# Kernel optimization log

Measured on AMD Instinct MI355X. Metric: run time of the kernel, lower is better.

Reference implementation:

```python
import jax, jax.numpy as jnp
import numpy as np

# ---- config (mirrors argparse-config of dnc_model) ----
T, B, IN = 64, 32, 64          # time-major input [T,B,IN]
N, Wd, R, NW = 512, 64, 4, 1   # memory_size, word_size, num_reads, num_writes
H, OUT = 256, 64               # controller hidden, output_size
CLIP = 20.0
EPS = 1e-6
IF = R*Wd + R + NW*Wd + NW + NW*Wd + NW*Wd + R + NW + NW + R*(1+2*NW)  # interface size = 471
CTRL_IN = IN + R*Wd


def setup_inputs() -> dict:
    key = jax.random.key(0)
    ks = jax.random.split(key, 6)
    g = lambda k, shape, s: (jax.random.normal(k, shape, jnp.float32) * s)
    return {
        "inputs": g(ks[0], (T, B, IN), 1.0),
        "Wx": g(ks[1], (CTRL_IN, 4*H), 0.05),
        "Wh": g(ks[2], (H, 4*H), 0.05),
        "b_lstm": jnp.zeros((4*H,), jnp.float32),
        "W_if": g(ks[3], (H, IF), 0.05),
        "b_if": jnp.zeros((IF,), jnp.float32),
        "W_out": g(ks[4], (H + R*Wd, OUT), 0.05),
        "b_out": jnp.zeros((OUT,), jnp.float32),
    }


def _clip(x):
    return jnp.clip(x, -CLIP, CLIP)


def _oneplus(x):
    return 1.0 + jax.nn.softplus(x)


def _content_weights(memory, keys, strengths):
    # memory [B,N,Wd], keys [B,K,Wd], strengths [B,K] -> softmax cosine weights [B,K,N]
    dot = jnp.einsum('bkw,bnw->bkn', keys, memory)
    mn = jnp.sqrt(jnp.sum(memory * memory, -1))          # [B,N]
    kn = jnp.sqrt(jnp.sum(keys * keys, -1))              # [B,K]
    sim = dot / (kn[..., None] * mn[:, None, :] + EPS)
    return jax.nn.softmax(sim * strengths[..., None], axis=-1)


def _allocation(usage):
    # usage [B,N] -> allocation weights [B,N] (sorted-free-list scheme)
    u = EPS + (1.0 - EPS) * usage
    idx = jnp.argsort(u, axis=-1)                        # ascending usage
    su = jnp.take_along_axis(u, idx, -1)
    cp = jnp.cumprod(su, axis=-1)
    excl = jnp.concatenate([jnp.ones_like(cp[:, :1]), cp[:, :-1]], -1)
    a_sorted = (1.0 - su) * excl
    inv = jnp.argsort(idx, axis=-1)
    return jnp.take_along_axis(a_sorted, inv, -1)


def _dnc_forward(inputs, Wx, Wh, b_lstm, W_if, b_if, W_out, b_out):
    eye = jnp.eye(N, dtype=inputs.dtype)

    def step(carry, x_t):
        h, c, mem, rw, ww_prev, link, prec, usage, reads = carry
        # ---- controller LSTM (prev read vectors fed in) ----
        ctrl_in = jnp.concatenate([x_t, reads.reshape(B, R*Wd)], -1)
        gates = ctrl_in @ Wx + h @ Wh + b_lstm
        ig, fg, gg, og = jnp.split(gates, 4, -1)
        c = jax.nn.sigmoid(fg) * c + jax.nn.sigmoid(ig) * jnp.tanh(gg)
        h = jax.nn.sigmoid(og) * jnp.tanh(c)
        hc, cc = _clip(h), _clip(c)
        # ---- interface vector ----
        itf = hc @ W_if + b_if
        off = 0
        read_keys = itf[:, off:off+R*Wd].reshape(B, R, Wd); off += R*Wd
        read_str = _oneplus(itf[:, off:off+R]); off += R
        write_keys = itf[:, off:off+NW*Wd].reshape(B, NW, Wd); off += NW*Wd
        write_str = _oneplus(itf[:, off:off+NW]); off += NW
        erase = jax.nn.sigmoid(itf[:, off:off+NW*Wd]).reshape(B, NW, Wd); off += NW*Wd
        write_vecs = itf[:, off:off+NW*Wd].reshape(B, NW, Wd); off += NW*Wd
        free_g = jax.nn.sigmoid(itf[:, off:off+R]); off += R
        alloc_g = jax.nn.sigmoid(itf[:, off:off+NW]); off += NW
        write_g = jax.nn.sigmoid(itf[:, off:off+NW]); off += NW
        modes = jax.nn.softmax(itf[:, off:off+R*(1+2*NW)].reshape(B, R, 1+2*NW), -1)
        bwd_mode = modes[..., :NW]
        fwd_mode = modes[..., NW:2*NW]
        content_mode = modes[..., 2*NW]
        # ---- usage update (uses prev write/read weights) ----
        u = usage + (1.0 - usage) * (1.0 - jnp.prod(1.0 - ww_prev, axis=1))
        psi = jnp.prod(1.0 - free_g[..., None] * rw, axis=1)
        usage = u * psi
        # ---- write weights: allocation + content ----
        allocs = []
        u_run = usage
        for hd in range(NW):
            a = _allocation(u_run)
            allocs.append(a)
            u_run = u_run + (1.0 - u_run) * (write_g[:, hd:hd+1] * alloc_g[:, hd:hd+1]) * a
        alloc = jnp.stack(allocs, 1)                      # [B,NW,N]
        wc = _content_weights(mem, write_keys, write_str) # [B,NW,N]
        ww = write_g[..., None] * (alloc_g[..., None] * alloc + (1.0 - alloc_g[..., None]) * wc)
        # ---- erase / add write ----
        erase_w = ww[..., None] * erase[:, :, None, :]    # [B,NW,N,Wd]
        mem = mem * jnp.prod(1.0 - erase_w, axis=1) + jnp.einsum('bhn,bhw->bnw', ww, write_vecs)
        # ---- temporal link + precedence ----
        w_i = ww[..., :, None]
        w_j = ww[..., None, :]
        link = (1.0 - w_i - w_j) * link + w_i * prec[..., None, :]
        link = link * (1.0 - eye)
        prec = (1.0 - ww.sum(-1, keepdims=True)) * prec + ww
        # ---- read weights: content + forward/backward linkage ----
        rc = _content_weights(mem, read_keys, read_str)   # [B,R,N]
        fw = jnp.einsum('bhij,brj->brhi', link, rw)       # forward  [B,R,NW,N]
        bw = jnp.einsum('bhji,brj->brhi', link, rw)       # backward [B,R,NW,N]
        rw = (content_mode[..., None] * rc
              + jnp.einsum('brh,brhn->brn', fwd_mode, fw)
              + jnp.einsum('brh,brhn->brn', bwd_mode, bw))
        reads = jnp.einsum('brn,bnw->brw', rw, mem)       # [B,R,Wd]
        out = _clip(jnp.concatenate([hc, reads.reshape(B, R*Wd)], -1) @ W_out + b_out)
        return (hc, cc, mem, rw, ww, link, prec, usage, reads), out

    z = jnp.zeros
    dt = inputs.dtype
    carry0 = (z((B, H), dt), z((B, H), dt), z((B, N, Wd), dt), z((B, R, N), dt),
              z((B, NW, N), dt), z((B, NW, N, N), dt), z((B, NW, N), dt),
              z((B, N), dt), z((B, R, Wd), dt))
    _, outs = jax.lax.scan(step, carry0, inputs)
    return outs  # [T, B, OUT]


def reference(inputs, Wx, Wh, b_lstm, W_if, b_if, W_out, b_out):
    return _dnc_forward(inputs, Wx, Wh, b_lstm, W_if, b_if, W_out, b_out)
```

## Files before the change

kernel.cpp:

```cpp
#include <hip/hip_runtime.h>
#include <math.h>

#define Tn 64
#define Bn 32
#define INn 64
#define Nn 512
#define WDn 64
#define Rn 4
#define Hn 256
#define G4H 1024
#define OUTn 64
#define IFn 471
#define CLIPV 20.0f
#define EPSV 1e-6f

#define OFF_RKEY 0
#define OFF_RSTR 256
#define OFF_WKEY 260
#define OFF_WSTR 324
#define OFF_ERASE 325
#define OFF_WVEC 389
#define OFF_FREE 453
#define OFF_AG 457
#define OFF_WG 458
#define OFF_MODES 459

__device__ float S_h[2][Bn][Hn];
__device__ float S_c[2][Bn][Hn];
__device__ float S_gates[2][Bn][G4H];
__device__ float S_mem[Bn][Nn][WDn];
__device__ float S_rw[Bn][Rn][Nn];
__device__ float S_ww[2][Bn][Nn];
__device__ float S_link[Bn][Nn][Nn];
__device__ float S_prec[2][Bn][Nn];
__device__ float S_usage[2][Bn][Nn];
__device__ float S_reads[Bn][Rn][WDn];
__device__ float S_itf[Bn][IFn];
__device__ float S_wsim[Bn][Nn];
__device__ float S_fw[Bn][Rn][Nn];
__device__ float S_bwp[Bn][8][Rn*Nn];
__device__ float S_sumww[Bn];
__device__ unsigned int g_hh[16];
__device__ unsigned int g_hb[Bn][16];
__device__ unsigned int g_itf[Bn][16];
__device__ unsigned int g_sim[Bn][16];
__device__ unsigned int g_ww[Bn][16];
__device__ unsigned int g_ld[Bn][16];
__device__ unsigned int g_fin[16];

__device__ __forceinline__ float sigm(float x){ return 1.f/(1.f+expf(-x)); }
__device__ __forceinline__ float clipv(float x){ return fminf(fmaxf(x,-CLIPV),CLIPV); }
__device__ __forceinline__ float oneplusf(float x){
  float sp = (x > 0.f) ? (x + log1pf(expf(-x))) : log1pf(expf(x));
  return 1.f + sp;
}
__device__ __forceinline__ float wredsum(float v){
  #pragma unroll
  for (int o=32;o>0;o>>=1) v += __shfl_xor(v,o,64);
  return v;
}
__device__ __forceinline__ float bredsum(float v, volatile float* scr){
  v = wredsum(v);
  if ((threadIdx.x & 63) == 0) scr[threadIdx.x >> 6] = v;
  __syncthreads();
  float s = scr[0];
  #pragma unroll
  for (int i=1;i<8;i++) s += scr[i];
  __syncthreads();
  return s;
}
__device__ __forceinline__ float bredmax(float v, volatile float* scr){
  #pragma unroll
  for (int o=32;o>0;o>>=1) v = fmaxf(v,__shfl_xor(v,o,64));
  if ((threadIdx.x & 63) == 0) scr[threadIdx.x >> 6] = v;
  __syncthreads();
  float m = scr[0];
  #pragma unroll
  for (int i=1;i<8;i++) m = fmaxf(m, scr[i]);
  __syncthreads();
  return m;
}
__device__ __forceinline__ void sig_release(unsigned int* flag){
  __builtin_amdgcn_fence(__ATOMIC_RELEASE, "agent");
  __hip_atomic_fetch_add(flag, 1u, __ATOMIC_RELAXED, __HIP_MEMORY_SCOPE_AGENT);
}
__device__ __forceinline__ void spin_until(unsigned int* flag, unsigned int target){
  while (__hip_atomic_load(flag, __ATOMIC_RELAXED, __HIP_MEMORY_SCOPE_AGENT) < target)
    __builtin_amdgcn_s_sleep(1);
}
__device__ __forceinline__ void wait_acq1(unsigned int* f, unsigned int tgt){
  if (threadIdx.x==0){
    spin_until(f, tgt);
    __builtin_amdgcn_fence(__ATOMIC_ACQUIRE, "agent");
  }
  __syncthreads();
}

extern "C" __global__ void __launch_bounds__(256)
k_init(){
  size_t g = (size_t)blockIdx.x*256 + threadIdx.x;
  size_t stride = (size_t)gridDim.x*256;
  float* lk = &S_link[0][0][0];
  for (size_t i=g; i<(size_t)Bn*Nn*Nn; i+=stride) lk[i]=0.f;
  float* mm = &S_mem[0][0][0];
  for (size_t i=g; i<(size_t)Bn*Nn*WDn; i+=stride) mm[i]=0.f;
  float* rr = &S_rw[0][0][0];
  for (size_t i=g; i<(size_t)Bn*Rn*Nn; i+=stride) rr[i]=0.f;
  float* rd = &S_reads[0][0][0];
  for (size_t i=g; i<(size_t)Bn*Rn*WDn; i+=stride) rd[i]=0.f;
  for (size_t i=g; i<(size_t)2*Bn*Nn; i+=stride){
    S_ww[0][0][i]=0.f; S_prec[0][0][i]=0.f; S_usage[0][0][i]=0.f;
  }
  for (size_t i=g; i<(size_t)2*Bn*Hn; i+=stride){
    S_h[0][0][i]=0.f; S_c[0][0][i]=0.f;
  }
  if (blockIdx.x==0){
    for (int i=threadIdx.x; i<16; i+=256){ g_hh[i]=0u; g_fin[i]=0u; }
    for (int i=threadIdx.x; i<Bn*16; i+=256){
      ((unsigned int*)g_hb)[i]=0u; ((unsigned int*)g_itf)[i]=0u;
      ((unsigned int*)g_sim)[i]=0u; ((unsigned int*)g_ww)[i]=0u;
      ((unsigned int*)g_ld)[i]=0u;
    }
  }
}

struct ShG { float ctrl[Bn][65]; };
struct ShAF {
  float itf[IFn];
  float ww[Nn];
  float red[8];
  float betar[Rn], knr[Rn], modes[Rn][4];
  float er[WDn], wv[WDn], rk[Rn][WDn];
  union {
    struct { unsigned long long keys[Nn]; float alloc[Nn]; float wsim[Nn]; } pre;
    struct {
      float tile[64][65];
      float rsim[Rn][Nn];
      float fw[Rn][Nn];
      float bw[Rn][Nn];
      float part[8][Rn][WDn];
      float vin[512];
    } post;
  } u;
};
struct ShL {
  float hc[Hn];
  float ipart[8][64];
  float wkey[WDn];
  float knw, betaw;
  float ww[Nn];
  float prec[Nn];
  float rw[Rn][Nn];
  float bwp4[4][Rn][Nn];
};
union ShU { ShAF a; ShL l; ShG g; };

extern "C" __global__ void __launch_bounds__(512)
k_gates_pro(const float* __restrict__ xin, const float* __restrict__ Wx,
            const float* __restrict__ Wh, const float* __restrict__ b_lstm){
  __shared__ ShG sg;
  const int tid = threadIdx.x, lane = tid & 63, wvi = tid >> 6;
  const int j = blockIdx.x*64 + lane;
  const int b0 = wvi*4;
  float bias = b_lstm[j];
  float a0=bias, a1=bias, a2=bias, a3=bias;
  {
    #pragma unroll
    for (int u=0;u<4;u++){
      int e = u*512 + tid;
      int b2 = e >> 6, kk = e & 63;
      sg.ctrl[b2][kk] = xin[(size_t)b2*INn + kk];
    }
    __syncthreads();
    const float* wb = Wx + j;
    #pragma unroll
    for (int kk=0;kk<64;kk++){
      float wv = wb[(size_t)kk*G4H];
      a0 += sg.ctrl[b0+0][kk]*wv;
      a1 += sg.ctrl[b0+1][kk]*wv;
      a2 += sg.ctrl[b0+2][kk]*wv;
      a3 += sg.ctrl[b0+3][kk]*wv;
    }
  }
  S_gates[0][b0+0][j]=a0;
  S_gates[0][b0+1][j]=a1;
  S_gates[0][b0+2][j]=a2;
  S_gates[0][b0+3][j]=a3;
}

extern "C" __global__ void __launch_bounds__(512, 4)
k_step(int t, const float* __restrict__ xin,
       const float* __restrict__ Wx, const float* __restrict__ Wh,
       const float* __restrict__ b_lstm,
       const float* __restrict__ W_if, const float* __restrict__ b_if,
       const float* __restrict__ W_out, const float* __restrict__ b_out,
       float* __restrict__ outp){
  __shared__ ShU sh;
  const int tid = threadIdx.x;
  const int lane = tid & 63, wvi = tid >> 6;
  const int bid = blockIdx.x;
  const int cur = t&1, prev = cur^1;

  if (bid < 32){
    const int b = bid;
    if (tid < Hn){
      int h = tid;
      float g0=S_gates[cur][b][h],     g1=S_gates[cur][b][Hn+h];
      float g2=S_gates[cur][b][2*Hn+h],g3=S_gates[cur][b][3*Hn+h];
      float cold = S_c[prev][b][h];
      float cn = sigm(g1)*cold + sigm(g0)*tanhf(g2);
      float hn = sigm(g3)*tanhf(cn);
      S_c[cur][b][h] = clipv(cn);
      S_h[cur][b][h] = clipv(hn);
    }
    __syncthreads();
    if (tid==0){ sig_release(&g_hb[b][0]); sig_release(&g_hh[0]); }
    wait_acq1(&g_itf[b][0], 8u*(unsigned)(t+1));
    for (int k=tid;k<IFn;k+=512) sh.a.itf[k] = S_itf[b][k];
    __syncthreads();
    if (tid < WDn){
      sh.a.er[tid] = sigm(sh.a.itf[OFF_ERASE+tid]);
      sh.a.wv[tid] = sh.a.itf[OFF_WVEC+tid];
    } else if (tid < WDn + Rn*WDn){
      int k2 = tid - WDn;
      sh.a.rk[k2>>6][k2&63] = sh.a.itf[OFF_RKEY + k2];
    } else if (tid < WDn + Rn*WDn + Rn){
      int r = tid - (WDn+Rn*WDn);
      sh.a.betar[r] = oneplusf(sh.a.itf[OFF_RSTR + r]);
    } else if (tid >= 384 && tid < 384+Rn){
      int r = tid - 384;
      float m0 = sh.a.itf[OFF_MODES + r*3 + 0];
      float m1 = sh.a.itf[OFF_MODES + r*3 + 1];
      float m2 = sh.a.itf[OFF_MODES + r*3 + 2];
      float mx = fmaxf(m0,fmaxf(m1,m2));
      float e0=expf(m0-mx), e1=expf(m1-mx), e2=expf(m2-mx);
      float si = e0+e1+e2;
      sh.a.modes[r][0]=e0/si; sh.a.modes[r][1]=e1/si; sh.a.modes[r][2]=e2/si;
    }
    {
      float fg0=sigm(sh.a.itf[OFF_FREE+0]), fg1=sigm(sh.a.itf[OFF_FREE+1]);
      float fg2=sigm(sh.a.itf[OFF_FREE+2]), fg3=sigm(sh.a.itf[OFF_FREE+3]);
      int n = tid;
      float uu = S_usage[prev][b][n], wwp = S_ww[prev][b][n];
      float u = uu + (1.f-uu)*wwp;
      float psi = (1.f - fg0*S_rw[b][0][n])*(1.f - fg1*S_rw[b][1][n])
                * (1.f - fg2*S_rw[b][2][n])*(1.f - fg3*S_rw[b][3][n]);
      float un = u*psi;
      S_usage[cur][b][n] = un;
      float v = EPSV + (1.f-EPSV)*un;
      sh.a.u.pre.keys[n] = ((unsigned long long)__float_as_uint(v) << 32) | (unsigned)n;
    }
    __syncthreads();
    if (wvi < 4){
      float kv = sh.a.rk[wvi][lane];
      float s2 = wredsum(kv*kv);
      if (lane==0) sh.a.knr[wvi] = sqrtf(s2);
    }
    {
      unsigned long long myk = sh.a.u.pre.keys[tid];
      float prod = 1.f;
      for (int j=0;j<Nn;j+=8){
        #pragma unroll
        for (int u=0;u<8;u++){
          unsigned long long kj = sh.a.u.pre.keys[j+u];
          float uj = __uint_as_float((unsigned)(kj>>32));
          prod *= (kj < myk) ? uj : 1.f;
        }
      }
      float myu = __uint_as_float((unsigned)(myk>>32));
      sh.a.u.pre.alloc[tid] = (1.f - myu)*prod;
    }
    wait_acq1(&g_sim[b][0], 8u*(unsigned)(t+1));
    sh.a.u.pre.wsim[tid] = S_wsim[b][tid];
    __syncthreads();
    {
      float v = sh.a.u.pre.wsim[tid];
      float mx = bredmax(v, sh.a.red);
      float e = expf(v - mx);
      float ssum = bredsum(e, sh.a.red);
      float wc = e/ssum;
      float ag = sigm(sh.a.itf[OFF_AG]);
      float wg = sigm(sh.a.itf[OFF_WG]);
      float wwv = wg*(ag*sh.a.u.pre.alloc[tid] + (1.f-ag)*wc);
      S_ww[cur][b][tid] = wwv;
      sh.a.ww[tid] = wwv;
      float wsum = bredsum(wwv, sh.a.red);
      if (tid==0) S_sumww[b] = wsum;
    }
    __syncthreads();
    if (tid==0) sig_release(&g_ww[b][0]);
    for (int tile=0;tile<8;tile++){
      #pragma unroll
      for (int u=0;u<8;u++){
        int e = u*512 + tid;
        int nn = e>>6, w = e&63;
        int n = tile*64+nn;
        float m = S_mem[b][n][w];
        float wwn = sh.a.ww[n];
        m = m*(1.f - wwn*sh.a.er[w]) + wwn*sh.a.wv[w];
        S_mem[b][n][w] = m;
        sh.a.u.post.tile[nn][w] = m;
      }
      __syncthreads();
      {
        int nn = tid>>3, qq = tid&7;
        float a0=0.f,a1=0.f,a2=0.f,a3=0.f,nrm=0.f;
        #pragma unroll
        for (int i=0;i<8;i++){
          int w = qq*8+i;
          float m = sh.a.u.post.tile[nn][w];
          a0 += m*sh.a.rk[0][w]; a1 += m*sh.a.rk[1][w];
          a2 += m*sh.a.rk[2][w]; a3 += m*sh.a.rk[3][w];
          nrm += m*m;
        }
        #pragma unroll
        for (int o=1;o<8;o<<=1){
          a0 += __shfl_xor(a0,o,64); a1 += __shfl_xor(a1,o,64);
          a2 += __shfl_xor(a2,o,64); a3 += __shfl_xor(a3,o,64);
          nrm += __shfl_xor(nrm,o,64);
        }
        if (qq==0){
          int n = tile*64+nn;
          float mn = sqrtf(nrm);
          sh.a.u.post.rsim[0][n] = sh.a.betar[0]*a0/(sh.a.knr[0]*mn + EPSV);
          sh.a.u.post.rsim[1][n] = sh.a.betar[1]*a1/(sh.a.knr[1]*mn + EPSV);
          sh.a.u.post.rsim[2][n] = sh.a.betar[2]*a2/(sh.a.knr[2]*mn + EPSV);
          sh.a.u.post.rsim[3][n] = sh.a.betar[3]*a3/(sh.a.knr[3]*mn + EPSV);
        }
      }
      __syncthreads();
    }
    for (int r=0;r<Rn;r++){
      float v = sh.a.u.post.rsim[r][tid];
      float mx = bredmax(v, sh.a.red);
      float e = expf(v - mx);
      float ssum = bredsum(e, sh.a.red);
      sh.a.u.post.rsim[r][tid] = e/ssum;
    }
    __syncthreads();
    wait_acq1(&g_ld[b][0], 8u*(unsigned)(t+1));
    for (int k=tid;k<Rn*Nn;k+=512){
      ((float*)sh.a.u.post.fw)[k] = ((const float*)S_fw[b])[k];
      float sbw = 0.f;
      #pragma unroll
      for (int ch=0;ch<8;ch++) sbw += S_bwp[b][ch][k];
      ((float*)sh.a.u.post.bw)[k] = sbw;
    }
    __syncthreads();
    for (int k=tid;k<Rn*Nn;k+=512){
      int r = k>>9, n = k&511;
      float v = sh.a.modes[r][2]*sh.a.u.post.rsim[r][n]
              + sh.a.modes[r][1]*sh.a.u.post.fw[r][n]
              + sh.a.modes[r][0]*sh.a.u.post.bw[r][n];
      sh.a.u.post.rsim[r][n] = v;
      S_rw[b][r][n] = v;
    }
    __syncthreads();
    {
      float a0=0.f,a1=0.f,a2=0.f,a3=0.f;
      #pragma unroll 4
      for (int nn=0;nn<64;nn++){
        int n = wvi*64+nn;
        float m = S_mem[b][n][lane];
        a0 += sh.a.u.post.rsim[0][n]*m; a1 += sh.a.u.post.rsim[1][n]*m;
        a2 += sh.a.u.post.rsim[2][n]*m; a3 += sh.a.u.post.rsim[3][n]*m;
      }
      sh.a.u.post.part[wvi][0][lane]=a0; sh.a.u.post.part[wvi][1][lane]=a1;
      sh.a.u.post.part[wvi][2][lane]=a2; sh.a.u.post.part[wvi][3][lane]=a3;
    }
    __syncthreads();
    if (tid < 256){
      int r = tid>>6, w = tid&63;
      float sv = 0.f;
      #pragma unroll
      for (int v=0;v<8;v++) sv += sh.a.u.post.part[v][r][w];
      S_reads[b][r][w] = sv;
      sh.a.u.post.vin[256+tid] = sv;
      sh.a.u.post.vin[tid] = S_h[cur][b][tid];
    }
    __syncthreads();
    {
      int qq = tid>>6, o = tid&63;
      float sacc = 0.f;
      for (int k2=qq*64;k2<qq*64+64;k2+=8){
        #pragma unroll
        for (int u=0;u<8;u++) sacc += sh.a.u.post.vin[k2+u]*W_out[(size_t)(k2+u)*OUTn + o];
      }
      sh.a.u.post.part[qq][0][o] = sacc;
    }
    __syncthreads();
    if (tid < 64){
      float sv = b_out[tid];
      #pragma unroll
      for (int qq=0;qq<8;qq++) sv += sh.a.u.post.part[qq][0][tid];
      outp[((size_t)t*Bn + b)*OUTn + tid] = clipv(sv);
    }
    __syncthreads();
    if (tid==0) sig_release(&g_fin[0]);

  } else if (bid < 288){
    const int idx = bid - 32;
    const int b = idx >> 3, ch = idx & 7;
    const int i0 = ch*64;
    wait_acq1(&g_hb[b][0], (unsigned)(t+1));
    if (tid < Hn) sh.l.hc[tid] = S_h[cur][b][tid];
    __syncthreads();
    const int col0 = ch*59;
    const int ncol = (col0+59 <= IFn) ? 59 : (IFn - col0);
    {
      float acc = 0.f;
      if (lane < ncol){
        const float* wp = W_if + (size_t)(wvi*32)*IFn + col0 + lane;
        #pragma unroll
        for (int kk=0;kk<32;kk++)
          acc += sh.l.hc[wvi*32+kk]*wp[(size_t)kk*IFn];
      }
      sh.l.ipart[wvi][lane] = acc;
    }
    __syncthreads();
    if (tid < ncol){
      float s = b_if[col0+tid];
      #pragma unroll
      for (int w=0;w<8;w++) s += sh.l.ipart[w][tid];
      S_itf[b][col0+tid] = s;
    }
    __syncthreads();
    if (tid==0) sig_release(&g_itf[b][0]);
    wait_acq1(&g_itf[b][0], 8u*(unsigned)(t+1));
    if (tid < WDn) sh.l.wkey[tid] = S_itf[b][OFF_WKEY+tid];
    else if (tid==64) sh.l.betaw = oneplusf(S_itf[b][OFF_WSTR]);
    __syncthreads();
    if (wvi==0){
      float kv = sh.l.wkey[lane];
      float s2 = wredsum(kv*kv);
      if (lane==0) sh.l.knw = sqrtf(s2);
    }
    __syncthreads();
    {
      int nn = tid>>3, qq = tid&7;
      int n = i0 + nn;
      const float4* mp = (const float4*)(&S_mem[b][n][qq*8]);
      float4 ma = mp[0], mb = mp[1];
      float d, nrm;
      {
        float k0=sh.l.wkey[qq*8+0], k1=sh.l.wkey[qq*8+1], k2=sh.l.wkey[qq*8+2], k3=sh.l.wkey[qq*8+3];
        float k4=sh.l.wkey[qq*8+4], k5=sh.l.wkey[qq*8+5], k6=sh.l.wkey[qq*8+6], k7=sh.l.wkey[qq*8+7];
        d   = ma.x*k0+ma.y*k1+ma.z*k2+ma.w*k3 + mb.x*k4+mb.y*k5+mb.z*k6+mb.w*k7;
        nrm = ma.x*ma.x+ma.y*ma.y+ma.z*ma.z+ma.w*ma.w
            + mb.x*mb.x+mb.y*mb.y+mb.z*mb.z+mb.w*mb.w;
      }
      #pragma unroll
      for (int o=1;o<8;o<<=1){ d += __shfl_xor(d,o,64); nrm += __shfl_xor(nrm,o,64); }
      if (qq==0)
        S_wsim[b][n] = sh.l.betaw * d / (sh.l.knw*sqrtf(nrm) + EPSV);
    }
    __syncthreads();
    if (tid==0) sig_release(&g_sim[b][0]);
    wait_acq1(&g_ww[b][0], (unsigned)(t+1));
    sh.l.ww[tid]   = S_ww[cur][b][tid];
    sh.l.prec[tid] = S_prec[prev][b][tid];
    for (int k=tid;k<Rn*Nn;k+=512) ((float*)sh.l.rw)[k] = ((const float*)S_rw[b])[k];
    __syncthreads();
    float sumww = S_sumww[b];
    float wj[2][4], pj[2][4], rj[4][2][4];
    #pragma unroll
    for (int jjc=0;jjc<2;jjc++){
      float4 w4 = ((const float4*)sh.l.ww)[jjc*64+lane];
      float4 p4 = ((const float4*)sh.l.prec)[jjc*64+lane];
      wj[jjc][0]=w4.x; wj[jjc][1]=w4.y; wj[jjc][2]=w4.z; wj[jjc][3]=w4.w;
      pj[jjc][0]=p4.x; pj[jjc][1]=p4.y; pj[jjc][2]=p4.z; pj[jjc][3]=p4.w;
      #pragma unroll
      for (int r=0;r<4;r++){
        float4 r4 = ((const float4*)sh.l.rw[r])[jjc*64+lane];
        rj[r][jjc][0]=r4.x; rj[r][jjc][1]=r4.y; rj[r][jjc][2]=r4.z; rj[r][jjc][3]=r4.w;
      }
    }
    float bwa[4][2][4];
    #pragma unroll
    for (int r=0;r<4;r++)
      #pragma unroll
      for (int jjc=0;jjc<2;jjc++)
        #pragma unroll
        for (int s=0;s<4;s++) bwa[r][jjc][s]=0.f;
    for (int rr=0;rr<8;rr++){
      const int i = i0 + wvi*8 + rr;
      float wi = sh.l.ww[i];
      float ci = 1.f - wi;
      float ri[4] = {sh.l.rw[0][i], sh.l.rw[1][i], sh.l.rw[2][i], sh.l.rw[3][i]};
      float f[4] = {0.f,0.f,0.f,0.f};
      float4* lrow4 = (float4*)(&S_link[b][i][0]);
      #pragma unroll
      for (int jjc=0;jjc<2;jjc++){
        float4 L4 = lrow4[jjc*64+lane];
        float Ls[4] = {L4.x, L4.y, L4.z, L4.w};
        #pragma unroll
        for (int s=0;s<4;s++){
          float Ln = (ci - wj[jjc][s])*Ls[s] + wi*pj[jjc][s];
          int j = jjc*256 + lane*4 + s;
          Ln = (j==i) ? 0.f : Ln;
          Ls[s] = Ln;
          #pragma unroll
          for (int r=0;r<4;r++){
            f[r] += Ln*rj[r][jjc][s];
            bwa[r][jjc][s] += Ln*ri[r];
          }
        }
        float4 Lo; Lo.x=Ls[0]; Lo.y=Ls[1]; Lo.z=Ls[2]; Lo.w=Ls[3];
        lrow4[jjc*64+lane] = Lo;
      }
      #pragma unroll
      for (int r=0;r<4;r++){
        float fr = wredsum(f[r]);
        if (lane==0) S_fw[b][r][i] = fr;
      }
    }
    if (wvi < 4){
      #pragma unroll
      for (int r=0;r<4;r++)
        #pragma unroll
        for (int jjc=0;jjc<2;jjc++){
          float4 v4; v4.x=bwa[r][jjc][0]; v4.y=bwa[r][jjc][1]; v4.z=bwa[r][jjc][2]; v4.w=bwa[r][jjc][3];
          ((float4*)sh.l.bwp4[wvi][r])[jjc*64+lane] = v4;
        }
    }
    __syncthreads();
    if (wvi >= 4){
      int v = wvi-4;
      #pragma unroll
      for (int r=0;r<4;r++)
        #pragma unroll
        for (int jjc=0;jjc<2;jjc++){
          float4 v4 = ((float4*)sh.l.bwp4[v][r])[jjc*64+lane];
          v4.x+=bwa[r][jjc][0]; v4.y+=bwa[r][jjc][1]; v4.z+=bwa[r][jjc][2]; v4.w+=bwa[r][jjc][3];
          ((float4*)sh.l.bwp4[v][r])[jjc*64+lane] = v4;
        }
    }
    __syncthreads();
    for (int k=tid;k<Rn*Nn;k+=512){
      float s = ((float*)sh.l.bwp4[0])[k] + ((float*)sh.l.bwp4[1])[k]
              + ((float*)sh.l.bwp4[2])[k] + ((float*)sh.l.bwp4[3])[k];
      S_bwp[b][ch][k] = s;
    }
    if (tid < 64){
      int j = i0 + tid;
      S_prec[cur][b][j] = (1.f - sumww)*sh.l.prec[j] + sh.l.ww[j];
    }
    __syncthreads();
    if (tid==0) sig_release(&g_ld[b][0]);

  } else {
    if (t+1 >= Tn) return;
    const int jt = bid - 288;
    const int j = jt*64 + lane;
    const int b0 = wvi*4;
    const int hp = cur;
    float bias = b_lstm[j];
    float a0=bias, a1=bias, a2=bias, a3=bias;
    wait_acq1(&g_hh[0], 32u*(unsigned)(t+1));
    for (int c=0;c<5;++c){
      #pragma unroll
      for (int u=0;u<4;u++){
        int e = u*512 + tid;
        int b2 = e >> 6, kk = e & 63;
        float v;
        if (c==0) v = xin[((size_t)(t+1)*Bn + b2)*INn + kk];
        else      v = S_h[hp][b2][(c-1)*64 + kk];
        sh.g.ctrl[b2][kk] = v;
      }
      __syncthreads();
      const float* wb = (c==0) ? (Wx + j)
                               : (Wh + (size_t)((c-1)*64)*G4H + j);
      #pragma unroll
      for (int kk=0;kk<64;kk++){
        float wv = wb[(size_t)kk*G4H];
        a0 += sh.g.ctrl[b0+0][kk]*wv;
        a1 += sh.g.ctrl[b0+1][kk]*wv;
        a2 += sh.g.ctrl[b0+2][kk]*wv;
        a3 += sh.g.ctrl[b0+3][kk]*wv;
      }
      __syncthreads();
    }
    wait_acq1(&g_fin[0], 32u*(unsigned)(t+1));
    for (int c=0;c<4;++c){
      #pragma unroll
      for (int u=0;u<4;u++){
        int e = u*512 + tid;
        int b2 = e >> 6, kk = e & 63;
        sh.g.ctrl[b2][kk] = ((const float*)S_reads[b2])[c*64 + kk];
      }
      __syncthreads();
      const float* wb = Wx + (size_t)(INn + c*64)*G4H + j;
      #pragma unroll
      for (int kk=0;kk<64;kk++){
        float wv = wb[(size_t)kk*G4H];
        a0 += sh.g.ctrl[b0+0][kk]*wv;
        a1 += sh.g.ctrl[b0+1][kk]*wv;
        a2 += sh.g.ctrl[b0+2][kk]*wv;
        a3 += sh.g.ctrl[b0+3][kk]*wv;
      }
      __syncthreads();
    }
    const int gs = (t+1)&1;
    S_gates[gs][b0+0][j]=a0;
    S_gates[gs][b0+1][j]=a1;
    S_gates[gs][b0+2][j]=a2;
    S_gates[gs][b0+3][j]=a3;
  }
}

extern "C" void kernel_launch(void* const* d_in, const int* in_sizes, int n_in,
                              void* d_out, int out_size, void* d_ws, size_t ws_size,
                              hipStream_t stream){
  (void)in_sizes; (void)n_in; (void)d_ws; (void)ws_size; (void)out_size;
  const float* xin = (const float*)d_in[0];
  const float* Wx  = (const float*)d_in[1];
  const float* Wh  = (const float*)d_in[2];
  const float* bl  = (const float*)d_in[3];
  const float* Wif = (const float*)d_in[4];
  const float* bif = (const float*)d_in[5];
  const float* Wo  = (const float*)d_in[6];
  const float* bo  = (const float*)d_in[7];
  hipLaunchKernelGGL(k_init, dim3(1024), dim3(256), 0, stream);
  hipLaunchKernelGGL(k_gates_pro, dim3(16), dim3(512), 0, stream, xin, Wx, Wh, bl);
  for (int t=0; t<Tn; ++t){
    hipLaunchKernelGGL(k_step, dim3(304), dim3(512), 0, stream,
                       t, xin, Wx, Wh, bl, Wif, bif, Wo, bo, (float*)d_out);
  }
}
```

Baseline: 6.271 ms.

## Move LSTM cell, interface, and write-weighting prep to the end of the previous step

Restructures the per-timestep schedule. The LSTM cell update, interface projection, usage/allocation, and write content similarity for step t+1 are now computed at the tail of step t in the per-batch blocks, after waiting on a new gate-ready flag. This removes several cross-block handshakes (hb, itf, sim, ww) and the separate link-block interface/similarity phases. A new prologue kernel computes the first step's controller and write weights. The cost is more serial work in the 32 batch blocks, which now compute the full interface matmul and similarity alone instead of splitting it across the link blocks.

```diff
diff --git a/kernel.cpp b/kernel.cpp
--- a/kernel.cpp
+++ b/kernel.cpp
@@ -36,17 +36,12 @@
 __device__ float S_usage[2][Bn][Nn];
 __device__ float S_reads[Bn][Rn][WDn];
 __device__ float S_itf[Bn][IFn];
-__device__ float S_wsim[Bn][Nn];
 __device__ float S_fw[Bn][Rn][Nn];
 __device__ float S_bwp[Bn][8][Rn*Nn];
 __device__ float S_sumww[Bn];
-__device__ unsigned int g_hh[16];
-__device__ unsigned int g_hb[Bn][16];
-__device__ unsigned int g_itf[Bn][16];
-__device__ unsigned int g_sim[Bn][16];
-__device__ unsigned int g_ww[Bn][16];
 __device__ unsigned int g_ld[Bn][16];
 __device__ unsigned int g_fin[16];
+__device__ unsigned int g_gate[16];
 
 __device__ __forceinline__ float sigm(float x){ return 1.f/(1.f+expf(-x)); }
 __device__ __forceinline__ float clipv(float x){ return fminf(fmaxf(x,-CLIPV),CLIPV); }
@@ -115,12 +110,8 @@
     S_h[0][0][i]=0.f; S_c[0][0][i]=0.f;
   }
   if (blockIdx.x==0){
-    for (int i=threadIdx.x; i<16; i+=256){ g_hh[i]=0u; g_fin[i]=0u; }
-    for (int i=threadIdx.x; i<Bn*16; i+=256){
-      ((unsigned int*)g_hb)[i]=0u; ((unsigned int*)g_itf)[i]=0u;
-      ((unsigned int*)g_sim)[i]=0u; ((unsigned int*)g_ww)[i]=0u;
-      ((unsigned int*)g_ld)[i]=0u;
-    }
+    for (int i=threadIdx.x; i<16; i+=256){ g_fin[i]=0u; g_gate[i]=0u; }
+    for (int i=threadIdx.x; i<Bn*16; i+=256) ((unsigned int*)g_ld)[i]=0u;
   }
 }
 
@@ -128,11 +119,14 @@
 struct ShAF {
   float itf[IFn];
   float ww[Nn];
+  float hc[Hn];
   float red[8];
   float betar[Rn], knr[Rn], modes[Rn][4];
   float er[WDn], wv[WDn], rk[Rn][WDn];
+  float wkey[WDn];
+  float knw;
   union {
-    struct { unsigned long long keys[Nn]; float alloc[Nn]; float wsim[Nn]; } pre;
+    struct { unsigned long long keys[Nn]; float alloc[Nn]; float wsim[Nn]; float tile[64][65]; } pre;
     struct {
       float tile[64][65];
       float rsim[Rn][Nn];
@@ -144,10 +138,6 @@
   } u;
 };
 struct ShL {
-  float hc[Hn];
-  float ipart[8][64];
-  float wkey[WDn];
-  float knw, betaw;
   float ww[Nn];
   float prec[Nn];
   float rw[Rn][Nn];
@@ -156,36 +146,71 @@
 union ShU { ShAF a; ShL l; ShG g; };
 
 extern "C" __global__ void __launch_bounds__(512)
-k_gates_pro(const float* __restrict__ xin, const float* __restrict__ Wx,
-            const float* __restrict__ Wh, const float* __restrict__ b_lstm){
-  __shared__ ShG sg;
-  const int tid = threadIdx.x, lane = tid & 63, wvi = tid >> 6;
-  const int j = blockIdx.x*64 + lane;
-  const int b0 = wvi*4;
-  float bias = b_lstm[j];
-  float a0=bias, a1=bias, a2=bias, a3=bias;
+k_pro(const float* __restrict__ xin, const float* __restrict__ Wx,
+      const float* __restrict__ b_lstm,
+      const float* __restrict__ W_if, const float* __restrict__ b_if){
+  __shared__ ShAF sh;
+  __shared__ float xs[64];
+  __shared__ float gv[G4H];
+  const int tid = threadIdx.x;
+  const int b = blockIdx.x;
+  if (tid<64) xs[tid] = xin[(size_t)b*INn + tid];
+  __syncthreads();
+  for (int o=tid;o<G4H;o+=512){
+    float acc = b_lstm[o];
+    #pragma unroll 8
+    for (int k=0;k<64;k++) acc += xs[k]*Wx[(size_t)k*G4H + o];
+    gv[o]=acc;
+  }
+  __syncthreads();
+  if (tid<Hn){
+    int h = tid;
+    float cn = sigm(gv[Hn+h])*0.f + sigm(gv[h])*tanhf(gv[2*Hn+h]);
+    float hn = sigm(gv[3*Hn+h])*tanhf(cn);
+    S_c[0][b][h] = clipv(cn);
+    float hv = clipv(hn);
+    S_h[0][b][h] = hv;
+    sh.hc[h] = hv;
+  }
+  __syncthreads();
+  if (tid < IFn){
+    float acc = b_if[tid];
+    for (int k=0;k<Hn;k+=16){
+      float s = 0.f;
+      #pragma unroll
+      for (int u=0;u<16;u++) s += sh.hc[k+u]*W_if[(size_t)(k+u)*IFn + tid];
+      acc += s;
+    }
+    sh.itf[tid] = acc;
+    S_itf[b][tid] = acc;
+  }
+  __syncthreads();
   {
-    #pragma unroll
-    for (int u=0;u<4;u++){
-      int e = u*512 + tid;
-      int b2 = e >> 6, kk = e & 63;
-      sg.ctrl[b2][kk] = xin[(size_t)b2*INn + kk];
-    }
-    __syncthreads();
-    const float* wb = Wx + j;
-    #pragma unroll
-    for (int kk=0;kk<64;kk++){
-      float wv = wb[(size_t)kk*G4H];
-      a0 += sg.ctrl[b0+0][kk]*wv;
-      a1 += sg.ctrl[b0+1][kk]*wv;
-      a2 += sg.ctrl[b0+2][kk]*wv;
-      a3 += sg.ctrl[b0+3][kk]*wv;
-    }
-  }
-  S_gates[0][b0+0][j]=a0;
-  S_gates[0][b0+1][j]=a1;
-  S_gates[0][b0+2][j]=a2;
-  S_gates[0][b0+3][j]=a3;
+    S_usage[0][b][tid] = 0.f;
+    sh.u.pre.keys[tid] = ((unsigned long long)__float_as_uint(EPSV) << 32) | (unsigned)tid;
+  }
+  __syncthreads();
+  {
+    unsigned long long myk = sh.u.pre.keys[tid];
+    float prod = 1.f;
+    for (int j=0;j<Nn;j+=8){
+      #pragma unroll
+      for (int u=0;u<8;u++){
+        unsigned long long kj = sh.u.pre.keys[j+u];
+        float uj = __uint_as_float((unsigned)(kj>>32));
+        prod *= (kj < myk) ? uj : 1.f;
+      }
+    }
+    float myu = __uint_as_float((unsigned)(myk>>32));
+    float alloc = (1.f - myu)*prod;
+    float wc = 1.f/512.f;
+    float ag = sigm(sh.itf[OFF_AG]);
+    float wg = sigm(sh.itf[OFF_WG]);
+    float wwv = wg*(ag*alloc + (1.f-ag)*wc);
+    S_ww[0][b][tid] = wwv;
+    float ws = bredsum(wwv, sh.red);
+    if (tid==0) S_sumww[b] = ws;
+  }
 }
 
 extern "C" __global__ void __launch_bounds__(512, 4)
@@ -203,20 +228,8 @@
 
   if (bid < 32){
     const int b = bid;
-    if (tid < Hn){
-      int h = tid;
-      float g0=S_gates[cur][b][h],     g1=S_gates[cur][b][Hn+h];
-      float g2=S_gates[cur][b][2*Hn+h],g3=S_gates[cur][b][3*Hn+h];
-      float cold = S_c[prev][b][h];
-      float cn = sigm(g1)*cold + sigm(g0)*tanhf(g2);
-      float hn = sigm(g3)*tanhf(cn);
-      S_c[cur][b][h] = clipv(cn);
-      S_h[cur][b][h] = clipv(hn);
-    }
-    __syncthreads();
-    if (tid==0){ sig_release(&g_hb[b][0]); sig_release(&g_hh[0]); }
-    wait_acq1(&g_itf[b][0], 8u*(unsigned)(t+1));
     for (int k=tid;k<IFn;k+=512) sh.a.itf[k] = S_itf[b][k];
+    sh.a.ww[tid] = S_ww[cur][b][tid];
     __syncthreads();
     if (tid < WDn){
       sh.a.er[tid] = sigm(sh.a.itf[OFF_ERASE+tid]);
@@ -237,58 +250,13 @@
       float si = e0+e1+e2;
       sh.a.modes[r][0]=e0/si; sh.a.modes[r][1]=e1/si; sh.a.modes[r][2]=e2/si;
     }
-    {
-      float fg0=sigm(sh.a.itf[OFF_FREE+0]), fg1=sigm(sh.a.itf[OFF_FREE+1]);
-      float fg2=sigm(sh.a.itf[OFF_FREE+2]), fg3=sigm(sh.a.itf[OFF_FREE+3]);
-      int n = tid;
-      float uu = S_usage[prev][b][n], wwp = S_ww[prev][b][n];
-      float u = uu + (1.f-uu)*wwp;
-      float psi = (1.f - fg0*S_rw[b][0][n])*(1.f - fg1*S_rw[b][1][n])
-                * (1.f - fg2*S_rw[b][2][n])*(1.f - fg3*S_rw[b][3][n]);
-      float un = u*psi;
-      S_usage[cur][b][n] = un;
-      float v = EPSV + (1.f-EPSV)*un;
-      sh.a.u.pre.keys[n] = ((unsigned long long)__float_as_uint(v) << 32) | (unsigned)n;
-    }
     __syncthreads();
     if (wvi < 4){
       float kv = sh.a.rk[wvi][lane];
       float s2 = wredsum(kv*kv);
       if (lane==0) sh.a.knr[wvi] = sqrtf(s2);
     }
-    {
-      unsigned long long myk = sh.a.u.pre.keys[tid];
-      float prod = 1.f;
-      for (int j=0;j<Nn;j+=8){
-        #pragma unroll
-        for (int u=0;u<8;u++){
-          unsigned long long kj = sh.a.u.pre.keys[j+u];
-          float uj = __uint_as_float((unsigned)(kj>>32));
-          prod *= (kj < myk) ? uj : 1.f;
-        }
-      }
-      float myu = __uint_as_float((unsigned)(myk>>32));
-      sh.a.u.pre.alloc[tid] = (1.f - myu)*prod;
-    }
-    wait_acq1(&g_sim[b][0], 8u*(unsigned)(t+1));
-    sh.a.u.pre.wsim[tid] = S_wsim[b][tid];
-    __syncthreads();
-    {
-      float v = sh.a.u.pre.wsim[tid];
-      float mx = bredmax(v, sh.a.red);
-      float e = expf(v - mx);
-      float ssum = bredsum(e, sh.a.red);
-      float wc = e/ssum;
-      float ag = sigm(sh.a.itf[OFF_AG]);
-      float wg = sigm(sh.a.itf[OFF_WG]);
-      float wwv = wg*(ag*sh.a.u.pre.alloc[tid] + (1.f-ag)*wc);
-      S_ww[cur][b][tid] = wwv;
-      sh.a.ww[tid] = wwv;
-      float wsum = bredsum(wwv, sh.a.red);
-      if (tid==0) S_sumww[b] = wsum;
-    }
-    __syncthreads();
-    if (tid==0) sig_release(&g_ww[b][0]);
+    __syncthreads();
     for (int tile=0;tile<8;tile++){
       #pragma unroll
       for (int u=0;u<8;u++){
@@ -398,65 +366,114 @@
     __syncthreads();
     if (tid==0) sig_release(&g_fin[0]);
 
+    if (t+1 < Tn){
+      wait_acq1(&g_gate[0], 16u*(unsigned)(t+1));
+      if (tid < Hn){
+        int h = tid;
+        float g0=S_gates[prev][b][h],     g1=S_gates[prev][b][Hn+h];
+        float g2=S_gates[prev][b][2*Hn+h],g3=S_gates[prev][b][3*Hn+h];
+        float cold = S_c[cur][b][h];
+        float cn = sigm(g1)*cold + sigm(g0)*tanhf(g2);
+        float hn = sigm(g3)*tanhf(cn);
+        S_c[prev][b][h] = clipv(cn);
+        float hv = clipv(hn);
+        S_h[prev][b][h] = hv;
+        sh.a.hc[h] = hv;
+      }
+      __syncthreads();
+      if (tid < IFn){
+        float acc = b_if[tid];
+        for (int k=0;k<Hn;k+=16){
+          float s = 0.f;
+          #pragma unroll
+          for (int u=0;u<16;u++) s += sh.a.hc[k+u]*W_if[(size_t)(k+u)*IFn + tid];
+          acc += s;
+        }
+        sh.a.itf[tid] = acc;
+        S_itf[b][tid] = acc;
+      }
+      __syncthreads();
+      if (tid < WDn) sh.a.wkey[tid] = sh.a.itf[OFF_WKEY+tid];
+      {
+        float fg0=sigm(sh.a.itf[OFF_FREE+0]), fg1=sigm(sh.a.itf[OFF_FREE+1]);
+        float fg2=sigm(sh.a.itf[OFF_FREE+2]), fg3=sigm(sh.a.itf[OFF_FREE+3]);
+        int n = tid;
+        float uu = S_usage[cur][b][n], wwp = sh.a.ww[n];
+        float u = uu + (1.f-uu)*wwp;
+        float psi = (1.f - fg0*S_rw[b][0][n])*(1.f - fg1*S_rw[b][1][n])
+                  * (1.f - fg2*S_rw[b][2][n])*(1.f - fg3*S_rw[b][3][n]);
+        float un = u*psi;
+        S_usage[prev][b][n] = un;
+        float v = EPSV + (1.f-EPSV)*un;
+        sh.a.u.pre.keys[n] = ((unsigned long long)__float_as_uint(v) << 32) | (unsigned)n;
+      }
+      __syncthreads();
+      if (wvi==0){
+        float kv = sh.a.wkey[lane];
+        float s2 = wredsum(kv*kv);
+        if (lane==0) sh.a.knw = sqrtf(s2);
+      }
+      {
+        unsigned long long myk = sh.a.u.pre.keys[tid];
+        float prod = 1.f;
+        for (int j=0;j<Nn;j+=8){
+          #pragma unroll
+          for (int u=0;u<8;u++){
+            unsigned long long kj = sh.a.u.pre.keys[j+u];
+            float uj = __uint_as_float((unsigned)(kj>>32));
+            prod *= (kj < myk) ? uj : 1.f;
+          }
+        }
+        float myu = __uint_as_float((unsigned)(myk>>32));
+        sh.a.u.pre.alloc[tid] = (1.f - myu)*prod;
+      }
+      __syncthreads();
+      float betaw = oneplusf(sh.a.itf[OFF_WSTR]);
+      for (int tile=0;tile<8;tile++){
+        #pragma unroll
+        for (int u=0;u<8;u++){
+          int e = u*512 + tid;
+          int nn = e>>6, w = e&63;
+          sh.a.u.pre.tile[nn][w] = S_mem[b][tile*64+nn][w];
+        }
+        __syncthreads();
+        {
+          int nn = tid>>3, qq = tid&7;
+          float d=0.f, nrm=0.f;
+          #pragma unroll
+          for (int i=0;i<8;i++){
+            int w = qq*8+i;
+            float m = sh.a.u.pre.tile[nn][w];
+            d += m*sh.a.wkey[w]; nrm += m*m;
+          }
+          #pragma unroll
+          for (int o=1;o<8;o<<=1){ d += __shfl_xor(d,o,64); nrm += __shfl_xor(nrm,o,64); }
+          if (qq==0){
+            int n = tile*64+nn;
+            sh.a.u.pre.wsim[n] = betaw * d / (sh.a.knw*sqrtf(nrm) + EPSV);
+          }
+        }
+        __syncthreads();
+      }
+      {
+        float v = sh.a.u.pre.wsim[tid];
+        float mx = bredmax(v, sh.a.red);
+        float e = expf(v - mx);
+        float ssum = bredsum(e, sh.a.red);
+        float wc = e/ssum;
+        float ag = sigm(sh.a.itf[OFF_AG]);
+        float wg = sigm(sh.a.itf[OFF_WG]);
+        float wwv = wg*(ag*sh.a.u.pre.alloc[tid] + (1.f-ag)*wc);
+        S_ww[prev][b][tid] = wwv;
+        float wsum = bredsum(wwv, sh.a.red);
+        if (tid==0) S_sumww[b] = wsum;
+      }
+    }
+
   } else if (bid < 288){
     const int idx = bid - 32;
     const int b = idx >> 3, ch = idx & 7;
     const int i0 = ch*64;
-    wait_acq1(&g_hb[b][0], (unsigned)(t+1));
-    if (tid < Hn) sh.l.hc[tid] = S_h[cur][b][tid];
-    __syncthreads();
-    const int col0 = ch*59;
-    const int ncol = (col0+59 <= IFn) ? 59 : (IFn - col0);
-    {
-      float acc = 0.f;
-      if (lane < ncol){
-        const float* wp = W_if + (size_t)(wvi*32)*IFn + col0 + lane;
-        #pragma unroll
-        for (int kk=0;kk<32;kk++)
-          acc += sh.l.hc[wvi*32+kk]*wp[(size_t)kk*IFn];
-      }
-      sh.l.ipart[wvi][lane] = acc;
-    }
-    __syncthreads();
-    if (tid < ncol){
-      float s = b_if[col0+tid];
-      #pragma unroll
-      for (int w=0;w<8;w++) s += sh.l.ipart[w][tid];
-      S_itf[b][col0+tid] = s;
-    }
-    __syncthreads();
-    if (tid==0) sig_release(&g_itf[b][0]);
-    wait_acq1(&g_itf[b][0], 8u*(unsigned)(t+1));
-    if (tid < WDn) sh.l.wkey[tid] = S_itf[b][OFF_WKEY+tid];
-    else if (tid==64) sh.l.betaw = oneplusf(S_itf[b][OFF_WSTR]);
-    __syncthreads();
-    if (wvi==0){
-      float kv = sh.l.wkey[lane];
-      float s2 = wredsum(kv*kv);
-      if (lane==0) sh.l.knw = sqrtf(s2);
-    }
-    __syncthreads();
-    {
-      int nn = tid>>3, qq = tid&7;
-      int n = i0 + nn;
-      const float4* mp = (const float4*)(&S_mem[b][n][qq*8]);
-      float4 ma = mp[0], mb = mp[1];
-      float d, nrm;
-      {
-        float k0=sh.l.wkey[qq*8+0], k1=sh.l.wkey[qq*8+1], k2=sh.l.wkey[qq*8+2], k3=sh.l.wkey[qq*8+3];
-        float k4=sh.l.wkey[qq*8+4], k5=sh.l.wkey[qq*8+5], k6=sh.l.wkey[qq*8+6], k7=sh.l.wkey[qq*8+7];
-        d   = ma.x*k0+ma.y*k1+ma.z*k2+ma.w*k3 + mb.x*k4+mb.y*k5+mb.z*k6+mb.w*k7;
-        nrm = ma.x*ma.x+ma.y*ma.y+ma.z*ma.z+ma.w*ma.w
-            + mb.x*mb.x+mb.y*mb.y+mb.z*mb.z+mb.w*mb.w;
-      }
-      #pragma unroll
-      for (int o=1;o<8;o<<=1){ d += __shfl_xor(d,o,64); nrm += __shfl_xor(nrm,o,64); }
-      if (qq==0)
-        S_wsim[b][n] = sh.l.betaw * d / (sh.l.knw*sqrtf(nrm) + EPSV);
-    }
-    __syncthreads();
-    if (tid==0) sig_release(&g_sim[b][0]);
-    wait_acq1(&g_ww[b][0], (unsigned)(t+1));
     sh.l.ww[tid]   = S_ww[cur][b][tid];
     sh.l.prec[tid] = S_prec[prev][b][tid];
     for (int k=tid;k<Rn*Nn;k+=512) ((float*)sh.l.rw)[k] = ((const float*)S_rw[b])[k];
@@ -553,10 +570,8 @@
     const int jt = bid - 288;
     const int j = jt*64 + lane;
     const int b0 = wvi*4;
-    const int hp = cur;
     float bias = b_lstm[j];
     float a0=bias, a1=bias, a2=bias, a3=bias;
-    wait_acq1(&g_hh[0], 32u*(unsigned)(t+1));
     for (int c=0;c<5;++c){
       #pragma unroll
       for (int u=0;u<4;u++){
@@ -564,7 +579,7 @@
         int b2 = e >> 6, kk = e & 63;
         float v;
         if (c==0) v = xin[((size_t)(t+1)*Bn + b2)*INn + kk];
-        else      v = S_h[hp][b2][(c-1)*64 + kk];
+        else      v = S_h[cur][b2][(c-1)*64 + kk];
         sh.g.ctrl[b2][kk] = v;
       }
       __syncthreads();
@@ -605,6 +620,8 @@
     S_gates[gs][b0+1][j]=a1;
     S_gates[gs][b0+2][j]=a2;
     S_gates[gs][b0+3][j]=a3;
+    __syncthreads();
+    if (tid==0) sig_release(&g_gate[0]);
   }
 }
 
@@ -621,7 +638,7 @@
   const float* Wo  = (const float*)d_in[6];
   const float* bo  = (const float*)d_in[7];
   hipLaunchKernelGGL(k_init, dim3(1024), dim3(256), 0, stream);
-  hipLaunchKernelGGL(k_gates_pro, dim3(16), dim3(512), 0, stream, xin, Wx, Wh, bl);
+  hipLaunchKernelGGL(k_pro, dim3(32), dim3(512), 0, stream, xin, Wx, bl, Wif, bif);
   for (int t=0; t<Tn; ++t){
     hipLaunchKernelGGL(k_step, dim3(304), dim3(512), 0, stream,
                        t, xin, Wx, Wh, bl, Wif, bif, Wo, bo, (float*)d_out);
```

Result: no change. 6.306 ms (+0.5%).
